# Kernel tuning notes

Hardware: AMD Instinct MI355X
Metric: run time of the kernel (lower is better)

## Reference

```python
import jax, jax.numpy as jnp
import numpy as np

H = 12
D_MODEL = 768
H_D = D_MODEL // H


def setup_inputs() -> dict:
    key = jax.random.key(0)
    ks = jax.random.split(key, 11)
    B, S = 2, 2048
    scale_in = 1.0
    w_scale = 1.0 / np.sqrt(D_MODEL)
    inp = {
        "query": jax.random.normal(ks[0], (B, S, D_MODEL), dtype=jnp.float32),
        "key": jax.random.normal(ks[1], (B, S, D_MODEL), dtype=jnp.float32),
        "value": jax.random.normal(ks[2], (B, S, D_MODEL), dtype=jnp.float32),
        "wq": jax.random.normal(ks[3], (D_MODEL, D_MODEL), dtype=jnp.float32) * w_scale,
        "bq": jnp.zeros((D_MODEL,), dtype=jnp.float32),
        "wk": jax.random.normal(ks[4], (D_MODEL, D_MODEL), dtype=jnp.float32) * w_scale,
        "bk": jnp.zeros((D_MODEL,), dtype=jnp.float32),
        "wv": jax.random.normal(ks[5], (D_MODEL, D_MODEL), dtype=jnp.float32) * w_scale,
        "bv": jnp.zeros((D_MODEL,), dtype=jnp.float32),
        "wo": jax.random.normal(ks[6], (D_MODEL, D_MODEL), dtype=jnp.float32) * w_scale,
        "bo": jnp.zeros((D_MODEL,), dtype=jnp.float32),
    }
    return inp


def reference(query, key, value, wq, bq, wk, bk, wv, bv, wo, bo):
    B, S, _ = query.shape
    # QKV projections, split into heads: [B, H, S, h_d]
    def proj(x, w, b):
        y = jnp.einsum("bsd,de->bse", x, w) + b
        return y.reshape(B, S, H, H_D).transpose(0, 2, 1, 3)

    q = proj(query, wq, bq)
    k = proj(key, wk, bk)
    v = proj(value, wv, bv)

    # scaled dot-product attention (dropout disabled / eval mode)
    scores = jnp.einsum("bhsd,bhtd->bhst", q, k) / jnp.sqrt(jnp.float32(H_D))
    wm = jax.nn.softmax(scores, axis=-1)  # [B, H, S, S]
    out = jnp.einsum("bhst,bhtd->bhsd", wm, v)

    # merge heads and output projection
    out = out.transpose(0, 2, 1, 3).reshape(B, S, D_MODEL)
    out = jnp.einsum("bsd,de->bse", out, wo) + bo
    return out
```

## Files before the change

kernel.cpp:

```cpp
#include <hip/hip_runtime.h>

#define H 12
#define DM 768
#define HD 64
#define SEQ 2048
#define BATCH 2
#define MROWS (BATCH*SEQ)

typedef __attribute__((ext_vector_type(8))) short short8;
typedef __attribute__((ext_vector_type(4))) float f32x4;
typedef __attribute__((ext_vector_type(16))) float f32x16;
using u16 = unsigned short;
using u32 = unsigned int;

__device__ __forceinline__ float bf2f(u16 u) { return __uint_as_float(((u32)u) << 16); }
__device__ __forceinline__ u16 f2bf(float x) {
  u32 u = __float_as_uint(x);
  return (u16)((u + 0x7fffu + ((u >> 16) & 1u)) >> 16);
}
__device__ __forceinline__ u32 cvt_pk_bf16(float lo, float hi) {
  u32 r;
  asm("v_cvt_pk_bf16_f32 %0, %1, %2" : "=v"(r) : "v"(lo), "v"(hi));
  return r;
}
__device__ __forceinline__ float fexp2(float x) {
  float r;
  asm("v_exp_f32 %0, %1" : "=v"(r) : "v"(x));
  return r;
}
__device__ __forceinline__ void gl2lds16(const u16* __restrict__ g, u16* l) {
  __builtin_amdgcn_global_load_lds(
      (const __attribute__((address_space(1))) unsigned int*)g,
      (__attribute__((address_space(3))) unsigned int*)l,
      16, 0, 0);
}

#define C_SM 0.18033688011112042f

__global__ __launch_bounds__(256) void transpose_w4(const float* __restrict__ w0, const float* __restrict__ w1,
                                                    const float* __restrict__ w2, const float* __restrict__ w3,
                                                    u16* __restrict__ dst0)
{
  __shared__ u16 Ts[64][72];
  const float* src = blockIdx.z == 0 ? w0 : blockIdx.z == 1 ? w1 : blockIdx.z == 2 ? w2 : w3;
  u16* dst = dst0 + (size_t)blockIdx.z * DM * DM;
  const int t = threadIdx.x;
  const int r0 = blockIdx.y * 64, c0 = blockIdx.x * 64;
  const int row = t >> 2, cq = (t & 3) * 16;
  const float* sp = src + (size_t)(r0 + row) * DM + c0 + cq;
  #pragma unroll
  for (int g = 0; g < 4; ++g) {
    float4 a = *reinterpret_cast<const float4*>(sp + g * 4);
    Ts[row][cq + g * 4 + 0] = f2bf(a.x);
    Ts[row][cq + g * 4 + 1] = f2bf(a.y);
    Ts[row][cq + g * 4 + 2] = f2bf(a.z);
    Ts[row][cq + g * 4 + 3] = f2bf(a.w);
  }
  __syncthreads();
  union { uint4 v[2]; u16 e[16]; } pk;
  #pragma unroll
  for (int j = 0; j < 16; ++j) pk.e[j] = Ts[cq + j][row];
  uint4* dp = reinterpret_cast<uint4*>(dst + (size_t)(c0 + row) * DM + r0 + cq);
  dp[0] = pk.v[0];
  dp[1] = pk.v[1];
}

template<int BM, bool AF32>
__device__ __forceinline__ void gemm_core(const void* __restrict__ Av, const u16* __restrict__ Bt,
                                          const float* __restrict__ bias, void* __restrict__ dstv,
                                          int mode, int bx, int by, float outScale)
{
  constexpr int AFR = BM / 32;
  constexpr int ACH = BM / 32;
  __shared__ u16 As[BM * 64];
  __shared__ u16 Bs[128 * 64];
  const int t = threadIdx.x;
  const int lane = t & 63, w = t >> 6;
  const int l15 = lane & 15, l4 = lane >> 4;
  const int m0 = by * BM, n0 = bx * 128;
  const int wr = (w >> 1) * (BM / 2), wc = (w & 1) * 64;

  f32x4 acc[AFR][4] = {};

  for (int kt = 0; kt < DM / 64; ++kt) {
    const int k0 = kt * 64;
    #pragma unroll
    for (int c = 0; c < ACH; ++c) {
      const int id = c * 256 + t;
      const int row = id >> 3, xc = id & 7;
      const int db = row * 128 + ((xc * 16) ^ ((row & 7) << 4));
      if (AF32) {
        const float* Af = reinterpret_cast<const float*>(Av) + (size_t)(m0 + row) * DM + k0 + xc * 8;
        float4 a0 = *reinterpret_cast<const float4*>(Af);
        float4 a1 = *reinterpret_cast<const float4*>(Af + 4);
        uint4 v;
        v.x = cvt_pk_bf16(a0.x, a0.y);
        v.y = cvt_pk_bf16(a0.z, a0.w);
        v.z = cvt_pk_bf16(a1.x, a1.y);
        v.w = cvt_pk_bf16(a1.z, a1.w);
        *reinterpret_cast<uint4*>(reinterpret_cast<char*>(As) + db) = v;
      } else {
        uint4 va = *reinterpret_cast<const uint4*>(reinterpret_cast<const u16*>(Av) +
                   (size_t)(m0 + row) * DM + k0 + xc * 8);
        *reinterpret_cast<uint4*>(reinterpret_cast<char*>(As) + db) = va;
      }
    }
    #pragma unroll
    for (int c = 0; c < 4; ++c) {
      const int id = c * 256 + t;
      const int row = id >> 3, xc = id & 7;
      const int db = row * 128 + ((xc * 16) ^ ((row & 7) << 4));
      uint4 vb = *reinterpret_cast<const uint4*>(Bt + (size_t)(n0 + row) * DM + k0 + xc * 8);
      *reinterpret_cast<uint4*>(reinterpret_cast<char*>(Bs) + db) = vb;
    }
    __syncthreads();
    #pragma unroll
    for (int ks = 0; ks < 2; ++ks) {
      short8 ag[AFR], bg[4];
      #pragma unroll
      for (int i = 0; i < AFR; ++i) {
        const int ar = wr + i * 16 + l15;
        ag[i] = *reinterpret_cast<const short8*>(reinterpret_cast<const char*>(As) +
                 ar * 128 + ((ks * 64 + l4 * 16) ^ ((ar & 7) << 4)));
      }
      #pragma unroll
      for (int j = 0; j < 4; ++j) {
        const int br = wc + j * 16 + l15;
        bg[j] = *reinterpret_cast<const short8*>(reinterpret_cast<const char*>(Bs) +
                 br * 128 + ((ks * 64 + l4 * 16) ^ ((br & 7) << 4)));
      }
      #pragma unroll
      for (int i = 0; i < AFR; ++i)
        #pragma unroll
        for (int j = 0; j < 4; ++j)
          acc[i][j] = __builtin_amdgcn_mfma_f32_16x16x32_bf16(ag[i], bg[j], acc[i][j], 0, 0, 0);
    }
    __syncthreads();
  }

  #pragma unroll
  for (int j = 0; j < 4; ++j) {
    const int gcol = n0 + wc + j * 16 + l15;
    const float bb = bias[gcol];
    #pragma unroll
    for (int i = 0; i < AFR; ++i) {
      const int grow = m0 + wr + i * 16 + l4 * 4;
      if (mode == 2) {
        float* dst = reinterpret_cast<float*>(dstv);
        #pragma unroll
        for (int r = 0; r < 4; ++r)
          dst[(size_t)(grow + r) * DM + gcol] = acc[i][j][r] + bb;
      } else {
        u16* dst = reinterpret_cast<u16*>(dstv);
        const int b = grow >> 11, s = grow & (SEQ - 1);
        const int h = gcol >> 6, d = gcol & 63;
        if (mode == 0) {
          #pragma unroll
          for (int r = 0; r < 4; ++r)
            dst[((size_t)(b * H + h) * SEQ + s + r) * HD + d] = f2bf((acc[i][j][r] + bb) * outScale);
        } else {
          union { uint2 v; u16 e[4]; } pk;
          #pragma unroll
          for (int r = 0; r < 4; ++r) pk.e[r] = f2bf(acc[i][j][r] + bb);
          *reinterpret_cast<uint2*>(dst + ((size_t)(b * H + h) * HD + d) * SEQ + s) = pk.v;
        }
      }
    }
  }
}

__device__ __forceinline__ void gemm_bf16(const u16* __restrict__ A, const u16* __restrict__ Bt,
                                          const float* __restrict__ bias, float* __restrict__ dst,
                                          int bx, int by)
{
  __shared__ u16 As[3][64 * 64];
  __shared__ u16 Bs[3][64 * 64];
  const int t = threadIdx.x;
  const int lane = t & 63, w = t >> 6;
  const int l15 = lane & 15, l4 = lane >> 4;
  const int m0 = by * 64, n0 = bx * 64;
  const int wr = (w >> 1) * 32, wc = (w & 1) * 32;
  constexpr int NK = DM / 64;
  const int r8 = lane >> 3;
  const int pcol = ((lane & 7) ^ r8) * 8;

  auto STAGE = [&](int kt2, int buf) {
    const int k0 = kt2 * 64;
    #pragma unroll
    for (int j = 0; j < 2; ++j) {
      const int ci = w * 2 + j;
      const int row = ci * 8 + r8;
      gl2lds16(A  + (size_t)(m0 + row) * DM + k0 + pcol, &As[buf][ci * 512]);
      gl2lds16(Bt + (size_t)(n0 + row) * DM + k0 + pcol, &Bs[buf][ci * 512]);
    }
  };

  STAGE(0, 0);
  STAGE(1, 1);

  f32x4 acc[2][2] = {};
  int cur = 0;

  for (int kt = 0; kt < NK; ++kt) {
    asm volatile("s_waitcnt vmcnt(4)" ::: "memory");
    __builtin_amdgcn_s_barrier();
    {
      int pt = kt + 2; if (pt >= NK) pt -= NK;
      STAGE(pt, cur == 0 ? 2 : cur - 1);
    }
    __builtin_amdgcn_s_setprio(1);
    #pragma unroll
    for (int ks = 0; ks < 2; ++ks) {
      short8 ag[2], bg[2];
      #pragma unroll
      for (int i = 0; i < 2; ++i) {
        const int ar = wr + i * 16 + l15;
        ag[i] = *reinterpret_cast<const short8*>(reinterpret_cast<const char*>(As[cur]) +
                 ar * 128 + ((ks * 64 + l4 * 16) ^ ((ar & 7) << 4)));
        const int br = wc + i * 16 + l15;
        bg[i] = *reinterpret_cast<const short8*>(reinterpret_cast<const char*>(Bs[cur]) +
                 br * 128 + ((ks * 64 + l4 * 16) ^ ((br & 7) << 4)));
      }
      #pragma unroll
      for (int i = 0; i < 2; ++i)
        #pragma unroll
        for (int j = 0; j < 2; ++j)
          acc[i][j] = __builtin_amdgcn_mfma_f32_16x16x32_bf16(ag[i], bg[j], acc[i][j], 0, 0, 0);
    }
    __builtin_amdgcn_s_setprio(0);
    cur = (cur == 2) ? 0 : cur + 1;
  }

  #pragma unroll
  for (int j = 0; j < 2; ++j) {
    const int gcol = n0 + wc + j * 16 + l15;
    const float bb = bias[gcol];
    #pragma unroll
    for (int i = 0; i < 2; ++i) {
      const int grow = m0 + wr + i * 16 + l4 * 4;
      #pragma unroll
      for (int r = 0; r < 4; ++r)
        dst[(size_t)(grow + r) * DM + gcol] = acc[i][j][r] + bb;
    }
  }
}

__global__ __launch_bounds__(256) void gemm_qkv_kernel(
    const float* __restrict__ xq, const float* __restrict__ xk, const float* __restrict__ xv,
    const u16* __restrict__ wT, const float* __restrict__ bq, const float* __restrict__ bk,
    const float* __restrict__ bv, u16* __restrict__ Qb, u16* __restrict__ Kb, u16* __restrict__ Vtb)
{
  const int flat = blockIdx.z * 384 + blockIdx.y * 6 + blockIdx.x;
  const int nb = (flat & 7) * 144 + (flat >> 3);
  const int z = nb / 384, rem = nb % 384;
  const int by = rem / 6, bx = rem % 6;
  const float* A    = z == 0 ? xq : z == 1 ? xk : xv;
  const u16* Bt     = wT + (size_t)z * DM * DM;
  const float* bias = z == 0 ? bq : z == 1 ? bk : bv;
  u16* dst          = z == 0 ? Qb : z == 1 ? Kb : Vtb;
  const float sc    = z == 1 ? C_SM : 1.0f;
  gemm_core<64, true>(A, Bt, bias, dst, z == 2 ? 1 : 0, bx, by, sc);
}

__global__ __launch_bounds__(256) void gemm_o_kernel(const u16* __restrict__ A, const u16* __restrict__ woT,
                                                     const float* __restrict__ bo, float* __restrict__ out)
{
  const int flat = blockIdx.y * 12 + blockIdx.x;
  const int nb = (flat & 7) * 96 + (flat >> 3);
  gemm_bf16(A, woT, bo, out, nb % 12, nb / 12);
}

__global__ __launch_bounds__(256) void attn_kernel(const u16* __restrict__ Q, const u16* __restrict__ K,
                                                   const u16* __restrict__ Vt,
                                                   float* __restrict__ Op0, float* __restrict__ Op1,
                                                   float* __restrict__ Lp0, float* __restrict__ Lp1)
{
  __shared__ u16 Ks[3][64 * 64];
  __shared__ u16 Vs[3][64 * 64];
  const int t = threadIdx.x;
  const int lane = t & 63, w = t >> 6;
  const int l31 = lane & 31, hi = lane >> 5;
  const int flat = blockIdx.y * 32 + blockIdx.x;
  const int nbid = (flat & 7) * 96 + (flat >> 3);
  const int bh = nbid >> 5;
  const int rem = nbid & 31;
  const int q0 = (rem >> 1) * 128;
  const int half = rem & 1;
  const int kv0 = half * (SEQ / 2);
  const size_t qbase  = ((size_t)bh * SEQ + q0) * HD;
  const size_t kbase0 = (size_t)bh * SEQ * HD;
  const size_t vtbase = (size_t)bh * HD * SEQ;
  float* __restrict__ Op = half ? Op1 : Op0;
  float* __restrict__ Lp = half ? Lp1 : Lp0;
  constexpr int NT = SEQ / 2 / 64;

  const int r8 = lane >> 3;
  const int pcol = ((lane & 7) ^ r8) * 8;

  short8 qf[4];
  {
    const u16* qp = Q + qbase + (size_t)(w * 32 + l31) * HD + hi * 8;
    #pragma unroll
    for (int ks = 0; ks < 4; ++ks)
      qf[ks] = *reinterpret_cast<const short8*>(qp + ks * 16);
  }

  auto STAGE = [&](int pt, int buf) {
    #pragma unroll
    for (int j = 0; j < 2; ++j) {
      const int ci = w * 2 + j;
      const int row = ci * 8 + r8;
      gl2lds16(K + kbase0 + (size_t)(kv0 + pt * 64 + row) * HD + pcol, &Ks[buf][ci * 512]);
      gl2lds16(Vt + vtbase + (size_t)row * SEQ + kv0 + pt * 64 + pcol, &Vs[buf][ci * 512]);
    }
  };

  STAGE(0, 0);
  STAGE(1, 1);

  short8 ones;
  #pragma unroll
  for (int j = 0; j < 8; ++j) ones[j] = (short)0x3F80;

  f32x16 oacc[2] = {};
  f32x16 accL = {};
  int cur = 0;

  for (int kt = 0; kt < NT; ++kt) {
    asm volatile("s_waitcnt vmcnt(4)" ::: "memory");
    __builtin_amdgcn_s_barrier();
    {
      const int pt = (kt + 2) & (NT - 1);
      const int pbuf = (cur + 2) % 3;
      STAGE(pt, pbuf);
    }

    f32x16 s0 = {}, s1 = {};
    __builtin_amdgcn_s_setprio(1);
    #pragma unroll
    for (int ks = 0; ks < 4; ++ks) {
      const int cb = ks * 32 + hi * 16;
      short8 kf0 = *reinterpret_cast<const short8*>(reinterpret_cast<const char*>(Ks[cur]) +
                   l31 * 128 + (cb ^ ((l31 & 7) << 4)));
      short8 kf1 = *reinterpret_cast<const short8*>(reinterpret_cast<const char*>(Ks[cur]) +
                   (32 + l31) * 128 + (cb ^ ((l31 & 7) << 4)));
      s0 = __builtin_amdgcn_mfma_f32_32x32x16_bf16(kf0, qf[ks], s0, 0, 0, 0);
      s1 = __builtin_amdgcn_mfma_f32_32x32x16_bf16(kf1, qf[ks], s1, 0, 0, 0);
    }
    __builtin_amdgcn_s_setprio(0);

    float p0[16], p1[16];
    #pragma unroll
    for (int r = 0; r < 16; ++r) {
      p0[r] = fexp2(s0[r]);
      p1[r] = fexp2(s1[r]);
    }

    __builtin_amdgcn_s_setprio(1);
    #pragma unroll
    for (int ks2 = 0; ks2 < 4; ++ks2) {
      const float* P = (ks2 < 2) ? p0 : p1;
      const int ro = (ks2 & 1) * 8;
      u32 a0 = cvt_pk_bf16(P[ro + 0], P[ro + 1]);
      u32 a1 = cvt_pk_bf16(P[ro + 2], P[ro + 3]);
      u32 b0 = cvt_pk_bf16(P[ro + 4], P[ro + 5]);
      u32 b1 = cvt_pk_bf16(P[ro + 6], P[ro + 7]);
      asm volatile("v_permlane32_swap_b32 %0, %1" : "+v"(a0), "+v"(b0));
      asm volatile("v_permlane32_swap_b32 %0, %1" : "+v"(a1), "+v"(b1));
      union { u32 u[4]; short8 s; } pa;
      pa.u[0] = a0; pa.u[1] = a1; pa.u[2] = b0; pa.u[3] = b1;
      accL = __builtin_amdgcn_mfma_f32_32x32x16_bf16(pa.s, ones, accL, 0, 0, 0);
      #pragma unroll
      for (int dt = 0; dt < 2; ++dt) {
        const int vr = dt * 32 + l31;
        short8 vf = *reinterpret_cast<const short8*>(reinterpret_cast<const char*>(Vs[cur]) +
                    vr * 128 + ((ks2 * 32 + hi * 16) ^ ((vr & 7) << 4)));
        oacc[dt] = __builtin_amdgcn_mfma_f32_32x32x16_bf16(pa.s, vf, oacc[dt], 0, 0, 0);
      }
    }
    __builtin_amdgcn_s_setprio(0);
    cur = (cur == 2) ? 0 : cur + 1;
  }

  if (l31 == 0) {
    #pragma unroll
    for (int r = 0; r < 16; ++r) {
      const int qo = (r & 3) + 8 * (r >> 2) + 4 * hi;
      Lp[(size_t)bh * SEQ + q0 + w * 32 + qo] = accL[r];
    }
  }
  #pragma unroll
  for (int r = 0; r < 16; ++r) {
    const int qo = (r & 3) + 8 * (r >> 2) + 4 * hi;
    const size_t base = ((size_t)bh * SEQ + q0 + w * 32 + qo) * HD;
    Op[base + l31]      = oacc[0][r];
    Op[base + 32 + l31] = oacc[1][r];
  }
}

__global__ __launch_bounds__(256) void attn_merge(const float* __restrict__ Op0, const float* __restrict__ Op1,
                                                  const float* __restrict__ Lp0, const float* __restrict__ Lp1,
                                                  u16* __restrict__ Ab)
{
  const int id = blockIdx.x * 256 + threadIdx.x;
  const int row = id >> 3, dc = (id & 7) * 8;
  const int bh = row >> 11, q = row & (SEQ - 1);
  const int b = bh / H, h = bh % H;
  const float inv = 1.f / (Lp0[row] + Lp1[row]);
  const float* p0 = Op0 + (size_t)row * HD + dc;
  const float* p1 = Op1 + (size_t)row * HD + dc;
  float4 a0 = *reinterpret_cast<const float4*>(p0);
  float4 a1 = *reinterpret_cast<const float4*>(p0 + 4);
  float4 c0 = *reinterpret_cast<const float4*>(p1);
  float4 c1 = *reinterpret_cast<const float4*>(p1 + 4);
  uint4 o;
  o.x = cvt_pk_bf16((a0.x + c0.x) * inv, (a0.y + c0.y) * inv);
  o.y = cvt_pk_bf16((a0.z + c0.z) * inv, (a0.w + c0.w) * inv);
  o.z = cvt_pk_bf16((a1.x + c1.x) * inv, (a1.y + c1.y) * inv);
  o.w = cvt_pk_bf16((a1.z + c1.z) * inv, (a1.w + c1.w) * inv);
  *reinterpret_cast<uint4*>(Ab + ((size_t)(b * SEQ + q)) * DM + h * HD + dc) = o;
}

extern "C" void kernel_launch(void* const* d_in, const int* in_sizes, int n_in,
                              void* d_out, int out_size, void* d_ws, size_t ws_size,
                              hipStream_t stream)
{
  const float* q  = (const float*)d_in[0];
  const float* k  = (const float*)d_in[1];
  const float* v  = (const float*)d_in[2];
  const float* wq = (const float*)d_in[3];
  const float* bq = (const float*)d_in[4];
  const float* wk = (const float*)d_in[5];
  const float* bk = (const float*)d_in[6];
  const float* wv = (const float*)d_in[7];
  const float* bv = (const float*)d_in[8];
  const float* wo = (const float*)d_in[9];
  const float* bo = (const float*)d_in[10];

  u16* ws = (u16*)d_ws;
  const size_t WSZ = (size_t)DM * DM;
  const size_t TSZ = (size_t)MROWS * DM;
  const size_t NQ  = (size_t)BATCH * H * SEQ;
  u16* wT  = ws;
  u16* Qb  = ws + 4 * WSZ;
  u16* Kb  = Qb + TSZ;
  u16* Vtb = Kb + TSZ;
  u16* Ab  = Vtb + TSZ;
  float* Op0 = (float*)(Ab + TSZ);
  float* Op1 = Op0 + TSZ;
  float* Lp0 = Op1 + TSZ;
  float* Lp1 = Lp0 + NQ;

  transpose_w4<<<dim3(12, 12, 4), 256, 0, stream>>>(wq, wk, wv, wo, wT);
  gemm_qkv_kernel<<<dim3(6, 64, 3), 256, 0, stream>>>(q, k, v, wT, bq, bk, bv, Qb, Kb, Vtb);
  attn_kernel<<<dim3(32, 24), 256, 0, stream>>>(Qb, Kb, Vtb, Op0, Op1, Lp0, Lp1);
  attn_merge<<<dim3((int)(NQ * 8 / 256)), 256, 0, stream>>>(Op0, Op1, Lp0, Lp1, Ab);
  gemm_o_kernel<<<dim3(12, 64), 256, 0, stream>>>(Ab, wT + 3 * WSZ, bo, (float*)d_out);
}
```

Before: 97.98 us.

## Software-pipeline QKV projection GEMM with register-prefetched A and async LDS B loads

```diff
diff --git a/kernel.cpp b/kernel.cpp
--- a/kernel.cpp
+++ b/kernel.cpp
@@ -65,77 +65,102 @@
   dp[1] = pk.v[1];
 }
 
-template<int BM, bool AF32>
-__device__ __forceinline__ void gemm_core(const void* __restrict__ Av, const u16* __restrict__ Bt,
-                                          const float* __restrict__ bias, void* __restrict__ dstv,
-                                          int mode, int bx, int by, float outScale)
-{
-  constexpr int AFR = BM / 32;
-  constexpr int ACH = BM / 32;
-  __shared__ u16 As[BM * 64];
-  __shared__ u16 Bs[128 * 64];
+__global__ __launch_bounds__(256) void gemm_qkv_kernel(
+    const float* __restrict__ xq, const float* __restrict__ xk, const float* __restrict__ xv,
+    const u16* __restrict__ wT, const float* __restrict__ bq, const float* __restrict__ bk,
+    const float* __restrict__ bv, u16* __restrict__ Qb, u16* __restrict__ Kb, u16* __restrict__ Vtb)
+{
+  const int flat = blockIdx.z * 384 + blockIdx.y * 6 + blockIdx.x;
+  const int nb = (flat & 7) * 144 + (flat >> 3);
+  const int z = nb / 384, rem = nb % 384;
+  const int by = rem / 6, bx = rem % 6;
+  const float* A    = z == 0 ? xq : z == 1 ? xk : xv;
+  const u16* Bt     = wT + (size_t)z * DM * DM;
+  const float* bias = z == 0 ? bq : z == 1 ? bk : bv;
+  u16* dst          = z == 0 ? Qb : z == 1 ? Kb : Vtb;
+  const int mode    = z == 2 ? 1 : 0;
+  const float outScale = z == 1 ? C_SM : 1.0f;
+
+  __shared__ u16 As[2][64 * 64];
+  __shared__ u16 Bs[3][64 * 128];
   const int t = threadIdx.x;
   const int lane = t & 63, w = t >> 6;
   const int l15 = lane & 15, l4 = lane >> 4;
-  const int m0 = by * BM, n0 = bx * 128;
-  const int wr = (w >> 1) * (BM / 2), wc = (w & 1) * 64;
-
-  f32x4 acc[AFR][4] = {};
-
-  for (int kt = 0; kt < DM / 64; ++kt) {
-    const int k0 = kt * 64;
-    #pragma unroll
-    for (int c = 0; c < ACH; ++c) {
-      const int id = c * 256 + t;
-      const int row = id >> 3, xc = id & 7;
-      const int db = row * 128 + ((xc * 16) ^ ((row & 7) << 4));
-      if (AF32) {
-        const float* Af = reinterpret_cast<const float*>(Av) + (size_t)(m0 + row) * DM + k0 + xc * 8;
-        float4 a0 = *reinterpret_cast<const float4*>(Af);
-        float4 a1 = *reinterpret_cast<const float4*>(Af + 4);
-        uint4 v;
-        v.x = cvt_pk_bf16(a0.x, a0.y);
-        v.y = cvt_pk_bf16(a0.z, a0.w);
-        v.z = cvt_pk_bf16(a1.x, a1.y);
-        v.w = cvt_pk_bf16(a1.z, a1.w);
-        *reinterpret_cast<uint4*>(reinterpret_cast<char*>(As) + db) = v;
-      } else {
-        uint4 va = *reinterpret_cast<const uint4*>(reinterpret_cast<const u16*>(Av) +
-                   (size_t)(m0 + row) * DM + k0 + xc * 8);
-        *reinterpret_cast<uint4*>(reinterpret_cast<char*>(As) + db) = va;
-      }
-    }
-    #pragma unroll
-    for (int c = 0; c < 4; ++c) {
-      const int id = c * 256 + t;
-      const int row = id >> 3, xc = id & 7;
-      const int db = row * 128 + ((xc * 16) ^ ((row & 7) << 4));
-      uint4 vb = *reinterpret_cast<const uint4*>(Bt + (size_t)(n0 + row) * DM + k0 + xc * 8);
-      *reinterpret_cast<uint4*>(reinterpret_cast<char*>(Bs) + db) = vb;
-    }
-    __syncthreads();
+  const int m0 = by * 64, n0 = bx * 128;
+  const int wr = (w >> 1) * 32, wc = (w & 1) * 64;
+  constexpr int NK = DM / 64;
+
+  const int arow = t >> 2, aseg = t & 3;
+  const int aswz = (arow & 7) << 4;
+  const int r8 = lane >> 3;
+  const int pcol = ((lane & 7) ^ r8) * 8;
+
+  float4 rA[2][4];
+  auto LOADA = [&](int kt2, int s) {
+    const float* Af = A + (size_t)(m0 + arow) * DM + kt2 * 64 + aseg * 16;
+    #pragma unroll
+    for (int i = 0; i < 4; ++i) rA[s][i] = *reinterpret_cast<const float4*>(Af + i * 4);
+  };
+  auto WRITEA = [&](int s, int buf) {
+    uint4 lo, hi;
+    lo.x = cvt_pk_bf16(rA[s][0].x, rA[s][0].y); lo.y = cvt_pk_bf16(rA[s][0].z, rA[s][0].w);
+    lo.z = cvt_pk_bf16(rA[s][1].x, rA[s][1].y); lo.w = cvt_pk_bf16(rA[s][1].z, rA[s][1].w);
+    hi.x = cvt_pk_bf16(rA[s][2].x, rA[s][2].y); hi.y = cvt_pk_bf16(rA[s][2].z, rA[s][2].w);
+    hi.z = cvt_pk_bf16(rA[s][3].x, rA[s][3].y); hi.w = cvt_pk_bf16(rA[s][3].z, rA[s][3].w);
+    char* base = reinterpret_cast<char*>(As[buf]) + arow * 128;
+    *reinterpret_cast<uint4*>(base + ((aseg * 32)      ^ aswz)) = lo;
+    *reinterpret_cast<uint4*>(base + ((aseg * 32 + 16) ^ aswz)) = hi;
+  };
+  auto ISSUEB = [&](int kt2, int buf) {
+    #pragma unroll
+    for (int j = 0; j < 4; ++j) {
+      const int ci = w * 4 + j;
+      const int row = ci * 8 + r8;
+      gl2lds16(Bt + (size_t)(n0 + row) * DM + kt2 * 64 + pcol, &Bs[buf][ci * 512]);
+    }
+  };
+
+  LOADA(0, 0); ISSUEB(0, 0);
+  LOADA(1, 1); ISSUEB(1, 1);
+
+  f32x4 acc[2][4] = {};
+
+  #pragma unroll
+  for (int kt = 0; kt < NK; ++kt) {
+    asm volatile("s_waitcnt vmcnt(8)" ::: "memory");
+    WRITEA(kt & 1, kt & 1);
+    asm volatile("s_waitcnt lgkmcnt(0)" ::: "memory");
+    __builtin_amdgcn_s_barrier();
+
+    {
+      int pt = kt + 2; if (pt >= NK) pt -= NK;
+      LOADA(pt, kt & 1);
+      ISSUEB(pt, (kt + 2) % 3);
+    }
+
+    __builtin_amdgcn_s_setprio(1);
     #pragma unroll
     for (int ks = 0; ks < 2; ++ks) {
-      short8 ag[AFR], bg[4];
-      #pragma unroll
-      for (int i = 0; i < AFR; ++i) {
+      short8 ag[2], bg[4];
+      #pragma unroll
+      for (int i = 0; i < 2; ++i) {
         const int ar = wr + i * 16 + l15;
-        ag[i] = *reinterpret_cast<const short8*>(reinterpret_cast<const char*>(As) +
+        ag[i] = *reinterpret_cast<const short8*>(reinterpret_cast<const char*>(As[kt & 1]) +
                  ar * 128 + ((ks * 64 + l4 * 16) ^ ((ar & 7) << 4)));
       }
       #pragma unroll
       for (int j = 0; j < 4; ++j) {
         const int br = wc + j * 16 + l15;
-        bg[j] = *reinterpret_cast<const short8*>(reinterpret_cast<const char*>(Bs) +
+        bg[j] = *reinterpret_cast<const short8*>(reinterpret_cast<const char*>(Bs[kt % 3]) +
                  br * 128 + ((ks * 64 + l4 * 16) ^ ((br & 7) << 4)));
       }
       #pragma unroll
-      for (int i = 0; i < AFR; ++i)
+      for (int i = 0; i < 2; ++i)
         #pragma unroll
         for (int j = 0; j < 4; ++j)
           acc[i][j] = __builtin_amdgcn_mfma_f32_16x16x32_bf16(ag[i], bg[j], acc[i][j], 0, 0, 0);
     }
-    __syncthreads();
+    __builtin_amdgcn_s_setprio(0);
   }
 
   #pragma unroll
@@ -143,27 +168,19 @@
     const int gcol = n0 + wc + j * 16 + l15;
     const float bb = bias[gcol];
     #pragma unroll
-    for (int i = 0; i < AFR; ++i) {
+    for (int i = 0; i < 2; ++i) {
       const int grow = m0 + wr + i * 16 + l4 * 4;
-      if (mode == 2) {
-        float* dst = reinterpret_cast<float*>(dstv);
+      const int b = grow >> 11, s = grow & (SEQ - 1);
+      const int h = gcol >> 6, d = gcol & 63;
+      if (mode == 0) {
         #pragma unroll
         for (int r = 0; r < 4; ++r)
-          dst[(size_t)(grow + r) * DM + gcol] = acc[i][j][r] + bb;
+          dst[((size_t)(b * H + h) * SEQ + s + r) * HD + d] = f2bf((acc[i][j][r] + bb) * outScale);
       } else {
-        u16* dst = reinterpret_cast<u16*>(dstv);
-        const int b = grow >> 11, s = grow & (SEQ - 1);
-        const int h = gcol >> 6, d = gcol & 63;
-        if (mode == 0) {
-          #pragma unroll
-          for (int r = 0; r < 4; ++r)
-            dst[((size_t)(b * H + h) * SEQ + s + r) * HD + d] = f2bf((acc[i][j][r] + bb) * outScale);
-        } else {
-          union { uint2 v; u16 e[4]; } pk;
-          #pragma unroll
-          for (int r = 0; r < 4; ++r) pk.e[r] = f2bf(acc[i][j][r] + bb);
-          *reinterpret_cast<uint2*>(dst + ((size_t)(b * H + h) * HD + d) * SEQ + s) = pk.v;
-        }
+        union { uint2 v; u16 e[4]; } pk;
+        #pragma unroll
+        for (int r = 0; r < 4; ++r) pk.e[r] = f2bf(acc[i][j][r] + bb);
+        *reinterpret_cast<uint2*>(dst + ((size_t)(b * H + h) * HD + d) * SEQ + s) = pk.v;
       }
     }
   }
@@ -243,23 +260,6 @@
         dst[(size_t)(grow + r) * DM + gcol] = acc[i][j][r] + bb;
     }
   }
-}
-
-__global__ __launch_bounds__(256) void gemm_qkv_kernel(
-    const float* __restrict__ xq, const float* __restrict__ xk, const float* __restrict__ xv,
-    const u16* __restrict__ wT, const float* __restrict__ bq, const float* __restrict__ bk,
-    const float* __restrict__ bv, u16* __restrict__ Qb, u16* __restrict__ Kb, u16* __restrict__ Vtb)
-{
-  const int flat = blockIdx.z * 384 + blockIdx.y * 6 + blockIdx.x;
-  const int nb = (flat & 7) * 144 + (flat >> 3);
-  const int z = nb / 384, rem = nb % 384;
-  const int by = rem / 6, bx = rem % 6;
-  const float* A    = z == 0 ? xq : z == 1 ? xk : xv;
-  const u16* Bt     = wT + (size_t)z * DM * DM;
-  const float* bias = z == 0 ? bq : z == 1 ? bk : bv;
-  u16* dst          = z == 0 ? Qb : z == 1 ? Kb : Vtb;
-  const float sc    = z == 1 ? C_SM : 1.0f;
-  gemm_core<64, true>(A, Bt, bias, dst, z == 2 ? 1 : 0, bx, by, sc);
 }
 
 __global__ __launch_bounds__(256) void gemm_o_kernel(const u16* __restrict__ A, const u16* __restrict__ woT,
```

After: 105.4 us. +7.6%, slower.
